# Kernel optimization log

Measured on AMD Instinct MI355X. Metric: run time of the kernel, lower is better.

## Reference

```python
import jax, jax.numpy as jnp
import numpy as np

VOCAB = 16000   # code_size
EMBED = 16
HID = 256
B, T = 64, 128


def _glorot(key, shape, fan):
    return jax.random.normal(key, shape, dtype=jnp.float32) / np.sqrt(fan)


def setup_inputs() -> dict:
    key = jax.random.key(0)
    ks = jax.random.split(key, 20)
    inp = {
        "tokens": jax.random.randint(ks[0], (B, T), 0, VOCAB),
        "h0": jax.random.normal(ks[1], (B, HID), dtype=jnp.float32),
        "c0": jax.random.normal(ks[2], (B, HID), dtype=jnp.float32),
        "emb": jax.random.normal(ks[3], (VOCAB, EMBED), dtype=jnp.float32),
        # LSTMCell params, PyTorch layout: W_ih [4H, in], W_hh [4H, H], biases [4H]
        "Wih1": _glorot(ks[4], (4 * HID, EMBED), EMBED),
        "Whh1": _glorot(ks[5], (4 * HID, HID), HID),
        "bih1": jnp.zeros((4 * HID,), jnp.float32),
        "bhh1": jnp.zeros((4 * HID,), jnp.float32),
        "Wih2": _glorot(ks[6], (4 * HID, HID), HID),
        "Whh2": _glorot(ks[7], (4 * HID, HID), HID),
        "bih2": jnp.zeros((4 * HID,), jnp.float32),
        "bhh2": jnp.zeros((4 * HID,), jnp.float32),
        "Wih3": _glorot(ks[8], (4 * HID, HID), HID),
        "Whh3": _glorot(ks[9], (4 * HID, HID), HID),
        "bih3": jnp.zeros((4 * HID,), jnp.float32),
        "bhh3": jnp.zeros((4 * HID,), jnp.float32),
        # head: Linear(HID,HID) -> ReLU -> Linear(HID,VOCAB)
        "W1": _glorot(ks[10], (HID, HID), HID),
        "b1": jnp.zeros((HID,), jnp.float32),
        "W2": _glorot(ks[11], (VOCAB, HID), HID),
        "b2": jnp.zeros((VOCAB,), jnp.float32),
    }
    return inp


def _lstm_cell(x, h, c, Wih, Whh, bih, bhh):
    # PyTorch LSTMCell gate order: i, f, g, o
    gates = x @ Wih.T + bih + h @ Whh.T + bhh          # [B, 4H]
    i, f, g, o = jnp.split(gates, 4, axis=-1)
    i, f, o = jax.nn.sigmoid(i), jax.nn.sigmoid(f), jax.nn.sigmoid(o)
    g = jnp.tanh(g)
    c_new = f * c + i * g
    h_new = o * jnp.tanh(c_new)
    return h_new, c_new


def reference(tokens, h0, c0, emb,
              Wih1, Whh1, bih1, bhh1,
              Wih2, Whh2, bih2, bhh2,
              Wih3, Whh3, bih3, bhh3,
              W1, b1, W2, b2):
    Bn, Tn = tokens.shape
    x = emb[tokens]                       # [B, T, E]
    xs = jnp.swapaxes(x, 0, 1)            # [T, B, E] for scan over time

    def step(carry, x_t):
        h1, c1, h2, c2, h3, c3 = carry
        h1, c1 = _lstm_cell(x_t, h1, c1, Wih1, Whh1, bih1, bhh1)
        h2, c2 = _lstm_cell(h1, h2, c2, Wih2, Whh2, bih2, bhh2)
        h3, c3 = _lstm_cell(h2, h3, c3, Wih3, Whh3, bih3, bhh3)
        score = jax.nn.relu(h3 @ W1.T + b1) @ W2.T + b2   # [B, V]
        return (h1, c1, h2, c2, h3, c3), score

    init = (h0, c0, h0, c0, h0, c0)       # hidden1 = hidden2 = hidden3 = hidden
    _, scores = jax.lax.scan(step, init, xs)              # [T, B, V]
    scores = jnp.swapaxes(scores, 0, 1).reshape(Bn * Tn, -1)
    labels = tokens.reshape(-1)
    return scores, labels
```

## Files before the change

### kernel.cpp

```cpp
#include <hip/hip_runtime.h>
#include <hip/hip_bf16.h>
#include <stdint.h>

#define T_SEQ 128
#define BATCH 64
#define HIDN  256
#define EMB   16
#define VOCAB 16000
#define HSTR  40
#define POIS  0x7FC1

typedef __attribute__((ext_vector_type(8))) short short8v;
typedef __attribute__((ext_vector_type(4))) float f32x4;
typedef __attribute__((ext_vector_type(4))) int   i32x4;
typedef unsigned short ushort_t;

#define OFF_WC1    0
#define OFF_WC2    131072
#define OFF_WC3    393216
#define OFF_BS2    655360
#define OFF_BS3    656384
#define OFF_W1BF   658432
#define OFF_H3     723968
#define OFF_S1     2821120
#define OFF_W2BF   3869696

#define OUT_XG     0
#define OUT_RINGS  8388608

#define RING_STRIDE 2113536
#define SLOT 16384

__device__ __forceinline__ ushort_t f2bf(float x) {
    __hip_bfloat16 h = __float2bfloat16(x);
    return *reinterpret_cast<ushort_t*>(&h);
}

__device__ __forceinline__ float dpp_x1(float x) {
    return __builtin_bit_cast(float, __builtin_amdgcn_mov_dpp(
        __builtin_bit_cast(int, x), 0xB1, 0xF, 0xF, true));
}
__device__ __forceinline__ float dpp_x2(float x) {
    return __builtin_bit_cast(float, __builtin_amdgcn_mov_dpp(
        __builtin_bit_cast(int, x), 0x4E, 0xF, 0xF, true));
}
__device__ __forceinline__ f32x4 dpp4_x1(f32x4 v) {
    f32x4 r; r[0]=dpp_x1(v[0]); r[1]=dpp_x1(v[1]); r[2]=dpp_x1(v[2]); r[3]=dpp_x1(v[3]); return r;
}
__device__ __forceinline__ f32x4 dpp4_x2(f32x4 v) {
    f32x4 r; r[0]=dpp_x2(v[0]); r[1]=dpp_x2(v[1]); r[2]=dpp_x2(v[2]); r[3]=dpp_x2(v[3]); return r;
}

__device__ __forceinline__ i32x4 bypass_ld128(const void* p) {
    i32x4 v;
    asm volatile("global_load_dwordx4 %0, %1, off sc0 sc1" : "=v"(v) : "v"((uint64_t)p));
    return v;
}
__device__ __forceinline__ void bypass_st128(void* p, f32x4 v) {
    asm volatile("global_store_dwordx4 %0, %1, off sc0 sc1" :: "v"((uint64_t)p), "v"(v) : "memory");
}
__device__ __forceinline__ void nt_st128(void* p, f32x4 v) {
    asm volatile("global_store_dwordx4 %0, %1, off nt" :: "v"((uint64_t)p), "v"(v) : "memory");
}
__device__ __forceinline__ void vm_drain() {
    asm volatile("s_waitcnt vmcnt(0)" ::: "memory");
    __builtin_amdgcn_sched_barrier(0);
}
__device__ __forceinline__ void lgkm_drain() {
    asm volatile("s_waitcnt lgkmcnt(0)" ::: "memory");
    __builtin_amdgcn_sched_barrier(0);
}

__global__ void k_poison(ushort_t* __restrict__ rbase) {
    unsigned int u = blockIdx.x * 256 + threadIdx.x;
    unsigned int l = u >> 20;
    unsigned int r = u & 1048575;
    unsigned int s = 1 + (r >> 13);
    unsigned int off = r & 8191;
    ((unsigned int*)(rbase + (size_t)l * RING_STRIDE + (size_t)s * SLOT))[off] = 0x7FC17FC1u;
}

__global__ void k_reorder_w(const float* __restrict__ Whh1,
                            const float* __restrict__ Wih2, const float* __restrict__ Whh2,
                            const float* __restrict__ Wih3, const float* __restrict__ Whh3,
                            float* __restrict__ wsf) {
    int bid = blockIdx.x;
    int layer = bid >> 10, c = bid & 1023;
    int wgi = c >> 7, rr = c & 127, jl = rr >> 2, gg = rr & 3;
    int row = gg * 256 + wgi * 32 + jl;
    int tid = threadIdx.x;
    if (layer == 0) {
        ushort_t* dst = (ushort_t*)(wsf + OFF_WC1) + (size_t)c * 256;
        dst[tid] = f2bf(Whh1[row * 256 + tid]);
    } else {
        const float* Wi = (layer == 1) ? Wih2 : Wih3;
        const float* Wh = (layer == 1) ? Whh2 : Whh3;
        ushort_t* dst = (ushort_t*)(wsf + ((layer == 1) ? OFF_WC2 : OFF_WC3)) + (size_t)c * 512;
        for (int k = tid; k < 512; k += 256)
            dst[k] = f2bf(k < 256 ? Wi[row * 256 + k] : Wh[row * 256 + k - 256]);
    }
}

__global__ void k_prep_small(const float* __restrict__ bi2, const float* __restrict__ bh2,
                             const float* __restrict__ bi3, const float* __restrict__ bh3,
                             const float* __restrict__ h0, const float* __restrict__ W1,
                             float* __restrict__ wsf, ushort_t* __restrict__ rbase) {
    int bid = blockIdx.x, tid = threadIdx.x;
    if (bid < 8) {
        int idx = bid * 256 + tid;
        int layer = idx >> 10, c = idx & 1023;
        int wgi = c >> 7, rr = c & 127, jl = rr >> 2, gg = rr & 3;
        int row = gg * 256 + wgi * 32 + jl;
        wsf[((layer == 0) ? OFF_BS2 : OFF_BS3) + c] =
            (layer == 0) ? (bi2[row] + bh2[row]) : (bi3[row] + bh3[row]);
    } else if (bid < 72) {
        int idx = (bid - 8) * 256 + tid;
        ushort_t v = f2bf(h0[idx]);
        rbase[idx] = v;
        rbase[RING_STRIDE + idx] = v;
        rbase[2 * RING_STRIDE + idx] = v;
    } else {
        int idx = (bid - 72) * 256 + tid;
        ((ushort_t*)(wsf + OFF_W1BF))[idx] = f2bf(W1[idx]);
    }
}

__global__ void k_xg(const int* __restrict__ tokens, const float* __restrict__ emb,
                     const float* __restrict__ Wih1, const float* __restrict__ bih1,
                     const float* __restrict__ bhh1, float* __restrict__ xg) {
    int t = blockIdx.x, cg = blockIdx.y;
    int tid = threadIdx.x;
    __shared__ float xs[64][16];
    for (int idx = tid; idx < 1024; idx += 256) {
        int b = idx >> 4, e = idx & 15;
        xs[b][e] = emb[(size_t)tokens[b * T_SEQ + t] * 16 + e];
    }
    __syncthreads();
    int c = cg * 64 + (tid & 63);
    int b0 = (tid >> 6) * 16;
    int wgi = c >> 7, rr = c & 127, jl = rr >> 2, gg = rr & 3;
    int row = gg * 256 + wgi * 32 + jl;
    float wv[16];
    #pragma unroll
    for (int e = 0; e < 16; ++e) wv[e] = Wih1[row * 16 + e];
    float bias = bih1[row] + bhh1[row];
    float* dst = xg + ((size_t)t * 1024 + c) * 64 + b0;
    for (int b = 0; b < 16; ++b) {
        float s = bias;
        #pragma unroll
        for (int e = 0; e < 16; ++e) s += xs[b0 + b][e] * wv[e];
        dst[b] = s;
    }
}

__global__ void k_conv_w2(const float* __restrict__ src, ushort_t* __restrict__ dst, int n8) {
    int idx = blockIdx.x * 256 + threadIdx.x;
    if (idx < n8) {
        f32x4 a = *(const f32x4*)(src + (size_t)idx * 8);
        f32x4 b = *(const f32x4*)(src + (size_t)idx * 8 + 4);
        short8v o;
        o[0] = (short)f2bf(a[0]); o[1] = (short)f2bf(a[1]);
        o[2] = (short)f2bf(a[2]); o[3] = (short)f2bf(a[3]);
        o[4] = (short)f2bf(b[0]); o[5] = (short)f2bf(b[1]);
        o[6] = (short)f2bf(b[2]); o[7] = (short)f2bf(b[3]);
        *(short8v*)(dst + (size_t)idx * 8) = o;
    }
}

template<int LAYER, int NKS>
__device__ __forceinline__ void lstm_body(
    int wg, int tid, const float* __restrict__ c0,
    float* __restrict__ wsf, float* __restrict__ outf,
    ushort_t* hA, ushort_t* hB, ushort_t* hS) {
    const int w = tid >> 6, lane = tid & 63, lr = lane & 15, lg = lane >> 4;
    const int g = lr & 3;
    const int K = NKS * 32;
    const ushort_t* WC = (const ushort_t*)(wsf + (LAYER == 0 ? OFF_WC1 : LAYER == 1 ? OFF_WC2 : OFF_WC3));
    ushort_t* H3b = (ushort_t*)(wsf + OFF_H3);
    const float* xg = outf + OUT_XG;
    ushort_t* rbase = (ushort_t*)(outf + OUT_RINGS);
    ushort_t* ringIn = rbase + (size_t)(LAYER == 0 ? 0 : LAYER - 1) * RING_STRIDE;
    ushort_t* ringOwn = rbase + (size_t)LAYER * RING_STRIDE;

    const int ccol = wg * 128 + 2 * w * 16 + lr;
    short8v wr0[NKS], wr1[NKS];
    #pragma unroll
    for (int ks = 0; ks < NKS; ++ks) {
        wr0[ks] = *(const short8v*)(WC + (size_t)ccol * K + ks * 32 + lg * 8);
        wr1[ks] = *(const short8v*)(WC + (size_t)(ccol + 16) * K + ks * 32 + lg * 8);
    }
    float bs0 = 0.f, bs1 = 0.f;
    if (LAYER > 0) {
        const float* BS = wsf + (LAYER == 1 ? OFF_BS2 : OFF_BS3);
        bs0 = BS[ccol]; bs1 = BS[ccol + 16];
    }
    const int jj0 = w * 8 + (lr >> 2);
    const int j0 = wg * 32 + jj0;
    f32x4 cst[4][2];
    #pragma unroll
    for (int i = 0; i < 4; ++i)
        #pragma unroll
        for (int r = 0; r < 4; ++r) {
            cst[i][0][r] = c0[(i * 16 + lg * 4 + r) * 256 + j0];
            cst[i][1][r] = c0[(i * 16 + lg * 4 + r) * 256 + j0 + 4];
        }

    const float sOwn = (g == 2) ? 2.f : -1.f;
    const float aOwn = (g == 2) ? -2.f : 1.f;
    const float bOwn = (g == 2) ? 1.f : 0.f;

    for (int t = 0; t < T_SEQ; ++t) {
        f32x4 xpre[8];
        if (LAYER == 0) {
            const float* xt = xg + ((size_t)t * 1024 + wg * 128) * 64;
            #pragma unroll
            for (int i = 0; i < 4; ++i) {
                xpre[i]     = *(const f32x4*)(xt + (size_t)(2 * w * 16 + lr) * 64 + i * 16 + lg * 4);
                xpre[i + 4] = *(const f32x4*)(xt + (size_t)((2 * w + 1) * 16 + lr) * 64 + i * 16 + lg * 4);
            }
        }
        i32x4 ta[8], tb[8];
        {
            const char* sA = (const char*)(LAYER == 0 ? (ringOwn + (size_t)t * SLOT)
                                                      : (ringIn + (size_t)(t + 1) * SLOT));
            const char* sB = (const char*)(ringOwn + (size_t)t * SLOT);
            bool bad;
            do {
                #pragma unroll
                for (int it = 0; it < 8; ++it)
                    ta[it] = bypass_ld128(sA + it * 4096 + tid * 16);
                if (LAYER > 0) {
                    #pragma unroll
                    for (int it = 0; it < 8; ++it)
                        tb[it] = bypass_ld128(sB + it * 4096 + tid * 16);
                }
                vm_drain();
                int p = 0;
                #pragma unroll
                for (int it = 0; it < 8; ++it)
                    p |= ((ta[it][0] & 0xFFFF) == POIS);
                if (LAYER > 0) {
                    #pragma unroll
                    for (int it = 0; it < 8; ++it)
                        p |= ((tb[it][0] & 0xFFFF) == POIS);
                }
                bad = __any(p);
            } while (bad);
        }
        __syncthreads();
        #pragma unroll
        for (int it = 0; it < 8; ++it) {
            int e16 = it * 256 + tid;
            int row = e16 >> 5, c16 = e16 & 31;
            int off = row * 512 + ((c16 ^ (row & 15)) << 4);
            *(i32x4*)((char*)hA + off) = ta[it];
            if (LAYER > 0) *(i32x4*)((char*)hB + off) = tb[it];
        }
        __syncthreads();
        f32x4 acc[4][2];
        if (LAYER == 0) {
            #pragma unroll
            for (int i = 0; i < 4; ++i) { acc[i][0] = xpre[i]; acc[i][1] = xpre[i + 4]; }
        } else {
            #pragma unroll
            for (int i = 0; i < 4; ++i) {
                acc[i][0] = (f32x4){bs0, bs0, bs0, bs0};
                acc[i][1] = (f32x4){bs1, bs1, bs1, bs1};
            }
        }
        #pragma unroll
        for (int i = 0; i < 4; ++i) {
            #pragma unroll
            for (int ks = 0; ks < NKS; ++ks) {
                const ushort_t* hsrc = (ks < 8) ? hA : hB;
                const int krem = ks & 7;
                short8v a = *(const short8v*)((const char*)hsrc + (i * 16 + lr) * 512 +
                                              (((krem * 4 + lg) ^ lr) << 4));
                acc[i][0] = __builtin_amdgcn_mfma_f32_16x16x32_bf16(a, wr0[ks], acc[i][0], 0, 0, 0);
                acc[i][1] = __builtin_amdgcn_mfma_f32_16x16x32_bf16(a, wr1[ks], acc[i][1], 0, 0, 0);
            }
        }
        #pragma unroll
        for (int i = 0; i < 4; ++i) {
            #pragma unroll
            for (int f = 0; f < 2; ++f) {
                f32x4 av = acc[i][f];
                f32x4 act;
                #pragma unroll
                for (int r = 0; r < 4; ++r) {
                    float e = __expf(sOwn * av[r]);
                    act[r] = fmaf(aOwn, __builtin_amdgcn_rcpf(1.f + e), bOwn);
                }
                f32x4 q1 = dpp4_x1(act), q2 = dpp4_x2(act), q3 = dpp4_x1(q2);
                f32x4 gI = (g == 0) ? act : (g == 1) ? q1 : (g == 2) ? q2 : q3;
                f32x4 gF = (g == 1) ? act : (g == 0) ? q1 : (g == 3) ? q2 : q3;
                f32x4 gG = (g == 2) ? act : (g == 3) ? q1 : (g == 0) ? q2 : q3;
                f32x4 gO = (g == 3) ? act : (g == 2) ? q1 : (g == 1) ? q2 : q3;
                f32x4 cv = gF * cst[i][f] + gI * gG;
                cst[i][f] = cv;
                float cg = (g == 0) ? cv[0] : (g == 1) ? cv[1] : (g == 2) ? cv[2] : cv[3];
                float go = (g == 0) ? gO[0] : (g == 1) ? gO[1] : (g == 2) ? gO[2] : gO[3];
                float e2 = __expf(2.f * cg);
                float th = fmaf(-2.f, __builtin_amdgcn_rcpf(1.f + e2), 1.f);
                float hval = go * th;
                int brow = i * 16 + lg * 4 + g;
                hS[brow * HSTR + jj0 + f * 4] = f2bf(hval);
            }
        }
        lgkm_drain();
        {
            f32x4 hv4 = *(const f32x4*)((const char*)hS + lane * (HSTR * 2) + w * 16);
            bypass_st128(ringOwn + (size_t)(t + 1) * SLOT + (size_t)lane * 256 + wg * 32 + w * 8, hv4);
            if (LAYER == 2)
                *(f32x4*)(H3b + (((size_t)lane * 128 + t) * 256 + wg * 32 + w * 8)) = hv4;
        }
    }
}

__global__ __launch_bounds__(256, 1) void k_lstm(const float* __restrict__ c0,
                                                 float* __restrict__ wsf,
                                                 float* __restrict__ outf) {
    __shared__ __align__(16) ushort_t hA[16384];
    __shared__ __align__(16) ushort_t hB[16384];
    __shared__ __align__(16) ushort_t hS[64 * HSTR];
    int layer = blockIdx.x >> 3, wg = blockIdx.x & 7;
    if (layer == 0)      lstm_body<0, 8>(wg, threadIdx.x, c0, wsf, outf, hA, hB, hS);
    else if (layer == 1) lstm_body<1, 16>(wg, threadIdx.x, c0, wsf, outf, hA, hB, hS);
    else                 lstm_body<2, 16>(wg, threadIdx.x, c0, wsf, outf, hA, hB, hS);
}

__global__ __launch_bounds__(256) void k_head1m(const ushort_t* __restrict__ H3,
                                                const ushort_t* __restrict__ W1B,
                                                const float* __restrict__ b1,
                                                ushort_t* __restrict__ S1) {
    __shared__ __align__(16) ushort_t As[128][32];
    __shared__ __align__(16) ushort_t Bs[128][32];
    int tid = threadIdx.x;
    int n0 = blockIdx.x * 128;
    int m0 = blockIdx.y * 128;
    int wave = tid >> 6, lane = tid & 63;
    int lr = lane & 15, lg = lane >> 4;
    int wm = (wave >> 1) * 64, wn = (wave & 1) * 64;
    f32x4 acc[4][4] = {};

    for (int kk = 0; kk < 256; kk += 32) {
        int id = tid;
        #pragma unroll
        for (int rep = 0; rep < 2; ++rep, id += 256) {
            int r = id >> 2, ch = (id & 3) * 8;
            *(short8v*)(&As[r][ch]) = *(const short8v*)(H3 + (size_t)(m0 + r) * 256 + kk + ch);
            *(short8v*)(&Bs[r][ch]) = *(const short8v*)(W1B + (size_t)(n0 + r) * 256 + kk + ch);
        }
        __syncthreads();
        short8v a[4], bb[4];
        #pragma unroll
        for (int i = 0; i < 4; ++i) a[i]  = *(const short8v*)(&As[wm + i * 16 + lr][lg * 8]);
        #pragma unroll
        for (int i = 0; i < 4; ++i) bb[i] = *(const short8v*)(&Bs[wn + i * 16 + lr][lg * 8]);
        #pragma unroll
        for (int i = 0; i < 4; ++i)
            #pragma unroll
            for (int f = 0; f < 4; ++f)
                acc[i][f] = __builtin_amdgcn_mfma_f32_16x16x32_bf16(a[i], bb[f], acc[i][f], 0, 0, 0);
        __syncthreads();
    }
    #pragma unroll
    for (int f = 0; f < 4; ++f) {
        int col = n0 + wn + f * 16 + lr;
        float bias = b1[col];
        #pragma unroll
        for (int i = 0; i < 4; ++i) {
            int rowb = m0 + wm + i * 16 + lg * 4;
            #pragma unroll
            for (int r = 0; r < 4; ++r)
                S1[(size_t)(rowb + r) * 256 + col] = f2bf(fmaxf(acc[i][f][r] + bias, 0.f));
        }
    }
}

__global__ __launch_bounds__(256) void k_head2(const ushort_t* __restrict__ S1,
                                               const ushort_t* __restrict__ W2,
                                               const float* __restrict__ b2, float* __restrict__ out) {
    __shared__ __align__(16) char smem[67584];
    ushort_t (*As)[32] = (ushort_t (*)[32])smem;
    ushort_t (*Bs)[32] = (ushort_t (*)[32])(smem + 8192);
    float* stage = (float*)smem;
    int tid = threadIdx.x;
    int n0 = blockIdx.x * 128;
    int m0 = blockIdx.y * 128;
    int wave = tid >> 6, lane = tid & 63;
    int lr = lane & 15, lg = lane >> 4;
    int wm = (wave >> 1) * 64, wn = (wave & 1) * 64;
    f32x4 acc[4][4] = {};

    for (int kk = 0; kk < 256; kk += 32) {
        int id = tid;
        #pragma unroll
        for (int rep = 0; rep < 2; ++rep, id += 256) {
            int r = id >> 2, ch = (id & 3) * 8;
            *(short8v*)(&As[r][ch]) = *(const short8v*)(S1 + (size_t)(m0 + r) * 256 + kk + ch);
            *(short8v*)(&Bs[r][ch]) = *(const short8v*)(W2 + (size_t)(n0 + r) * 256 + kk + ch);
        }
        __syncthreads();
        short8v a[4], bb[4];
        #pragma unroll
        for (int i = 0; i < 4; ++i) a[i]  = *(const short8v*)(&As[wm + i * 16 + lr][lg * 8]);
        #pragma unroll
        for (int i = 0; i < 4; ++i) bb[i] = *(const short8v*)(&Bs[wn + i * 16 + lr][lg * 8]);
        #pragma unroll
        for (int i = 0; i < 4; ++i)
            #pragma unroll
            for (int f = 0; f < 4; ++f)
                acc[i][f] = __builtin_amdgcn_mfma_f32_16x16x32_bf16(a[i], bb[f], acc[i][f], 0, 0, 0);
        __syncthreads();
    }
    #pragma unroll
    for (int f = 0; f < 4; ++f) {
        int col = wn + f * 16 + lr;
        float bias = b2[n0 + col];
        #pragma unroll
        for (int i = 0; i < 4; ++i) {
            int rowl = wm + i * 16 + lg * 4;
            #pragma unroll
            for (int r = 0; r < 4; ++r)
                stage[(rowl + r) * 132 + col] = acc[i][f][r] + bias;
        }
    }
    __syncthreads();
    #pragma unroll
    for (int j = 0; j < 16; ++j) {
        int idx = j * 256 + tid;
        int row = idx >> 5, c4 = idx & 31;
        f32x4 v = *(const f32x4*)(stage + row * 132 + c4 * 4);
        nt_st128(out + (size_t)(m0 + row) * VOCAB + n0 + c4 * 4, v);
    }
}

__global__ void k_labels(const int* __restrict__ tokens, float* __restrict__ out) {
    int i = blockIdx.x * 256 + threadIdx.x;
    if (i < BATCH * T_SEQ) out[i] = (float)tokens[i];
}

extern "C" void kernel_launch(void* const* d_in, const int* in_sizes, int n_in,
                              void* d_out, int out_size, void* d_ws, size_t ws_size,
                              hipStream_t stream) {
    const int*   tokens = (const int*)d_in[0];
    const float* h0   = (const float*)d_in[1];
    const float* c0   = (const float*)d_in[2];
    const float* emb  = (const float*)d_in[3];
    const float* Wih1 = (const float*)d_in[4];
    const float* Whh1 = (const float*)d_in[5];
    const float* bih1 = (const float*)d_in[6];
    const float* bhh1 = (const float*)d_in[7];
    const float* Wih2 = (const float*)d_in[8];
    const float* Whh2 = (const float*)d_in[9];
    const float* bih2 = (const float*)d_in[10];
    const float* bhh2 = (const float*)d_in[11];
    const float* Wih3 = (const float*)d_in[12];
    const float* Whh3 = (const float*)d_in[13];
    const float* bih3 = (const float*)d_in[14];
    const float* bhh3 = (const float*)d_in[15];
    const float* W1   = (const float*)d_in[16];
    const float* b1   = (const float*)d_in[17];
    const float* W2   = (const float*)d_in[18];
    const float* b2   = (const float*)d_in[19];

    float* ws  = (float*)d_ws;
    float* out = (float*)d_out;

    k_poison<<<12288, 256, 0, stream>>>((ushort_t*)(out + OUT_RINGS));
    k_reorder_w<<<3072, 256, 0, stream>>>(Whh1, Wih2, Whh2, Wih3, Whh3, ws);
    k_prep_small<<<328, 256, 0, stream>>>(bih2, bhh2, bih3, bhh3, h0, W1,
                                          ws, (ushort_t*)(out + OUT_RINGS));
    k_xg<<<dim3(128, 16), 256, 0, stream>>>(tokens, emb, Wih1, bih1, bhh1, out + OUT_XG);
    k_conv_w2<<<2000, 256, 0, stream>>>(W2, (ushort_t*)(ws + OFF_W2BF), VOCAB * 256 / 8);

    k_lstm<<<24, 256, 0, stream>>>(c0, ws, out);

    dim3 g1(2, 64);
    k_head1m<<<g1, 256, 0, stream>>>((const ushort_t*)(ws + OFF_H3),
                                     (const ushort_t*)(ws + OFF_W1BF), b1,
                                     (ushort_t*)(ws + OFF_S1));
    dim3 g2(125, 64);
    k_head2<<<g2, 256, 0, stream>>>((const ushort_t*)(ws + OFF_S1),
                                    (const ushort_t*)(ws + OFF_W2BF), b2, out);
    k_labels<<<32, 256, 0, stream>>>(tokens, out + (size_t)BATCH * T_SEQ * VOCAB);
}
```

Before: 1.091 ms.

## Split LSTM timestep into two batch halves to pipeline ring handoff

Each timestep's work in the persistent LSTM kernel is split into two phases over batch halves (rows 0-31 and 32-63). Each phase polls and loads only its half of the ring slot, computes its gates and publishes its half of h immediately. The downstream layer and the next step can then start on the first half while the second is still being computed, which shortens the serial critical path across layers. In exchange there are twice as many spin-poll rounds and __syncthreads barriers per step, and half the lanes sit idle during each publish.

```diff
diff --git a/kernel.cpp b/kernel.cpp
--- a/kernel.cpp
+++ b/kernel.cpp
@@ -30,6 +30,7 @@
 
 #define RING_STRIDE 2113536
 #define SLOT 16384
+#define HALF_B 16384
 
 __device__ __forceinline__ ushort_t f2bf(float x) {
     __hip_bfloat16 h = __float2bfloat16(x);
@@ -210,109 +211,116 @@
     const float bOwn = (g == 2) ? 1.f : 0.f;
 
     for (int t = 0; t < T_SEQ; ++t) {
-        f32x4 xpre[8];
-        if (LAYER == 0) {
-            const float* xt = xg + ((size_t)t * 1024 + wg * 128) * 64;
-            #pragma unroll
-            for (int i = 0; i < 4; ++i) {
-                xpre[i]     = *(const f32x4*)(xt + (size_t)(2 * w * 16 + lr) * 64 + i * 16 + lg * 4);
-                xpre[i + 4] = *(const f32x4*)(xt + (size_t)((2 * w + 1) * 16 + lr) * 64 + i * 16 + lg * 4);
-            }
-        }
-        i32x4 ta[8], tb[8];
-        {
-            const char* sA = (const char*)(LAYER == 0 ? (ringOwn + (size_t)t * SLOT)
-                                                      : (ringIn + (size_t)(t + 1) * SLOT));
-            const char* sB = (const char*)(ringOwn + (size_t)t * SLOT);
-            bool bad;
-            do {
+        #pragma unroll
+        for (int ph = 0; ph < 2; ++ph) {
+            f32x4 xp0[2], xp1[2];
+            if (LAYER == 0) {
+                const float* xt = xg + ((size_t)t * 1024 + wg * 128) * 64;
                 #pragma unroll
-                for (int it = 0; it < 8; ++it)
-                    ta[it] = bypass_ld128(sA + it * 4096 + tid * 16);
-                if (LAYER > 0) {
+                for (int il = 0; il < 2; ++il) {
+                    int i = ph * 2 + il;
+                    xp0[il] = *(const f32x4*)(xt + (size_t)(2 * w * 16 + lr) * 64 + i * 16 + lg * 4);
+                    xp1[il] = *(const f32x4*)(xt + (size_t)((2 * w + 1) * 16 + lr) * 64 + i * 16 + lg * 4);
+                }
+            }
+            i32x4 ta[4], tb[4];
+            {
+                const char* sA = (const char*)(LAYER == 0 ? (ringOwn + (size_t)t * SLOT)
+                                                          : (ringIn + (size_t)(t + 1) * SLOT)) + ph * HALF_B;
+                const char* sB = (const char*)(ringOwn + (size_t)t * SLOT) + ph * HALF_B;
+                bool bad;
+                do {
                     #pragma unroll
-                    for (int it = 0; it < 8; ++it)
-                        tb[it] = bypass_ld128(sB + it * 4096 + tid * 16);
+                    for (int it = 0; it < 4; ++it)
+                        ta[it] = bypass_ld128(sA + it * 4096 + tid * 16);
+                    if (LAYER > 0) {
+                        #pragma unroll
+                        for (int it = 0; it < 4; ++it)
+                            tb[it] = bypass_ld128(sB + it * 4096 + tid * 16);
+                    }
+                    vm_drain();
+                    int p = 0;
+                    #pragma unroll
+                    for (int it = 0; it < 4; ++it)
+                        p |= ((ta[it][0] & 0xFFFF) == POIS);
+                    if (LAYER > 0) {
+                        #pragma unroll
+                        for (int it = 0; it < 4; ++it)
+                            p |= ((tb[it][0] & 0xFFFF) == POIS);
+                    }
+                    bad = __any(p);
+                } while (bad);
+            }
+            __syncthreads();
+            #pragma unroll
+            for (int it = 0; it < 4; ++it) {
+                int e16 = it * 256 + tid;
+                int row = ph * 32 + (e16 >> 5), c16 = e16 & 31;
+                int off = row * 512 + ((c16 ^ (row & 15)) << 4);
+                *(i32x4*)((char*)hA + off) = ta[it];
+                if (LAYER > 0) *(i32x4*)((char*)hB + off) = tb[it];
+            }
+            __syncthreads();
+            f32x4 acc[2][2];
+            if (LAYER == 0) {
+                #pragma unroll
+                for (int il = 0; il < 2; ++il) { acc[il][0] = xp0[il]; acc[il][1] = xp1[il]; }
+            } else {
+                #pragma unroll
+                for (int il = 0; il < 2; ++il) {
+                    acc[il][0] = (f32x4){bs0, bs0, bs0, bs0};
+                    acc[il][1] = (f32x4){bs1, bs1, bs1, bs1};
                 }
-                vm_drain();
-                int p = 0;
+            }
+            #pragma unroll
+            for (int il = 0; il < 2; ++il) {
+                int i = ph * 2 + il;
                 #pragma unroll
-                for (int it = 0; it < 8; ++it)
-                    p |= ((ta[it][0] & 0xFFFF) == POIS);
-                if (LAYER > 0) {
+                for (int ks = 0; ks < NKS; ++ks) {
+                    const ushort_t* hsrc = (ks < 8) ? hA : hB;
+                    const int krem = ks & 7;
+                    short8v a = *(const short8v*)((const char*)hsrc + (i * 16 + lr) * 512 +
+                                                  (((krem * 4 + lg) ^ lr) << 4));
+                    acc[il][0] = __builtin_amdgcn_mfma_f32_16x16x32_bf16(a, wr0[ks], acc[il][0], 0, 0, 0);
+                    acc[il][1] = __builtin_amdgcn_mfma_f32_16x16x32_bf16(a, wr1[ks], acc[il][1], 0, 0, 0);
+                }
+            }
+            #pragma unroll
+            for (int il = 0; il < 2; ++il) {
+                int i = ph * 2 + il;
+                #pragma unroll
+                for (int f = 0; f < 2; ++f) {
+                    f32x4 av = acc[il][f];
+                    f32x4 act;
                     #pragma unroll
-                    for (int it = 0; it < 8; ++it)
-                        p |= ((tb[it][0] & 0xFFFF) == POIS);
+                    for (int r = 0; r < 4; ++r) {
+                        float e = __expf(sOwn * av[r]);
+                        act[r] = fmaf(aOwn, __builtin_amdgcn_rcpf(1.f + e), bOwn);
+                    }
+                    f32x4 q1 = dpp4_x1(act), q2 = dpp4_x2(act), q3 = dpp4_x1(q2);
+                    f32x4 gI = (g == 0) ? act : (g == 1) ? q1 : (g == 2) ? q2 : q3;
+                    f32x4 gF = (g == 1) ? act : (g == 0) ? q1 : (g == 3) ? q2 : q3;
+                    f32x4 gG = (g == 2) ? act : (g == 3) ? q1 : (g == 0) ? q2 : q3;
+                    f32x4 gO = (g == 3) ? act : (g == 2) ? q1 : (g == 1) ? q2 : q3;
+                    f32x4 cv = gF * cst[i][f] + gI * gG;
+                    cst[i][f] = cv;
+                    float cg = (g == 0) ? cv[0] : (g == 1) ? cv[1] : (g == 2) ? cv[2] : cv[3];
+                    float go = (g == 0) ? gO[0] : (g == 1) ? gO[1] : (g == 2) ? gO[2] : gO[3];
+                    float e2 = __expf(2.f * cg);
+                    float th = fmaf(-2.f, __builtin_amdgcn_rcpf(1.f + e2), 1.f);
+                    float hval = go * th;
+                    int brow = i * 16 + lg * 4 + g;
+                    hS[brow * HSTR + jj0 + f * 4] = f2bf(hval);
                 }
-                bad = __any(p);
-            } while (bad);
-        }
-        __syncthreads();
-        #pragma unroll
-        for (int it = 0; it < 8; ++it) {
-            int e16 = it * 256 + tid;
-            int row = e16 >> 5, c16 = e16 & 31;
-            int off = row * 512 + ((c16 ^ (row & 15)) << 4);
-            *(i32x4*)((char*)hA + off) = ta[it];
-            if (LAYER > 0) *(i32x4*)((char*)hB + off) = tb[it];
-        }
-        __syncthreads();
-        f32x4 acc[4][2];
-        if (LAYER == 0) {
-            #pragma unroll
-            for (int i = 0; i < 4; ++i) { acc[i][0] = xpre[i]; acc[i][1] = xpre[i + 4]; }
-        } else {
-            #pragma unroll
-            for (int i = 0; i < 4; ++i) {
-                acc[i][0] = (f32x4){bs0, bs0, bs0, bs0};
-                acc[i][1] = (f32x4){bs1, bs1, bs1, bs1};
-            }
-        }
-        #pragma unroll
-        for (int i = 0; i < 4; ++i) {
-            #pragma unroll
-            for (int ks = 0; ks < NKS; ++ks) {
-                const ushort_t* hsrc = (ks < 8) ? hA : hB;
-                const int krem = ks & 7;
-                short8v a = *(const short8v*)((const char*)hsrc + (i * 16 + lr) * 512 +
-                                              (((krem * 4 + lg) ^ lr) << 4));
-                acc[i][0] = __builtin_amdgcn_mfma_f32_16x16x32_bf16(a, wr0[ks], acc[i][0], 0, 0, 0);
-                acc[i][1] = __builtin_amdgcn_mfma_f32_16x16x32_bf16(a, wr1[ks], acc[i][1], 0, 0, 0);
-            }
-        }
-        #pragma unroll
-        for (int i = 0; i < 4; ++i) {
-            #pragma unroll
-            for (int f = 0; f < 2; ++f) {
-                f32x4 av = acc[i][f];
-                f32x4 act;
-                #pragma unroll
-                for (int r = 0; r < 4; ++r) {
-                    float e = __expf(sOwn * av[r]);
-                    act[r] = fmaf(aOwn, __builtin_amdgcn_rcpf(1.f + e), bOwn);
-                }
-                f32x4 q1 = dpp4_x1(act), q2 = dpp4_x2(act), q3 = dpp4_x1(q2);
-                f32x4 gI = (g == 0) ? act : (g == 1) ? q1 : (g == 2) ? q2 : q3;
-                f32x4 gF = (g == 1) ? act : (g == 0) ? q1 : (g == 3) ? q2 : q3;
-                f32x4 gG = (g == 2) ? act : (g == 3) ? q1 : (g == 0) ? q2 : q3;
-                f32x4 gO = (g == 3) ? act : (g == 2) ? q1 : (g == 1) ? q2 : q3;
-                f32x4 cv = gF * cst[i][f] + gI * gG;
-                cst[i][f] = cv;
-                float cg = (g == 0) ? cv[0] : (g == 1) ? cv[1] : (g == 2) ? cv[2] : cv[3];
-                float go = (g == 0) ? gO[0] : (g == 1) ? gO[1] : (g == 2) ? gO[2] : gO[3];
-                float e2 = __expf(2.f * cg);
-                float th = fmaf(-2.f, __builtin_amdgcn_rcpf(1.f + e2), 1.f);
-                float hval = go * th;
-                int brow = i * 16 + lg * 4 + g;
-                hS[brow * HSTR + jj0 + f * 4] = f2bf(hval);
-            }
-        }
-        lgkm_drain();
-        {
-            f32x4 hv4 = *(const f32x4*)((const char*)hS + lane * (HSTR * 2) + w * 16);
-            bypass_st128(ringOwn + (size_t)(t + 1) * SLOT + (size_t)lane * 256 + wg * 32 + w * 8, hv4);
-            if (LAYER == 2)
-                *(f32x4*)(H3b + (((size_t)lane * 128 + t) * 256 + wg * 32 + w * 8)) = hv4;
+            }
+            lgkm_drain();
+            if (lane < 32) {
+                int brow = ph * 32 + lane;
+                f32x4 hv4 = *(const f32x4*)((const char*)hS + brow * (HSTR * 2) + w * 16);
+                bypass_st128(ringOwn + (size_t)(t + 1) * SLOT + (size_t)brow * 256 + wg * 32 + w * 8, hv4);
+                if (LAYER == 2)
+                    *(f32x4*)(H3b + (((size_t)brow * 128 + t) * 256 + wg * 32 + w * 8)) = hv4;
+            }
         }
     }
 }
```

Measured after the change: 1.148 ms. 5.3% more time.
